# Kernel optimization log

Measured on AMD Instinct MI355X. Metric: run time of the kernel, lower is better.

## Reference

```python
import jax, jax.numpy as jnp
import numpy as np

N = 200_000
E = 6_400_000
EPS = 1e-12


def l2_normalize(x):
    # F.normalize(x, p=2, dim=1): x / max(||x||_2, eps)
    n = jnp.linalg.norm(x, axis=1, keepdims=True)
    return x / jnp.maximum(n, EPS)


def gcn_conv(x, W, b, src, dst, n):
    """PyG GCNConv: add self-loops, symmetric normalization D^-1/2 A D^-1/2,
    linear transform (no bias) on nodes, scatter-add to targets, then + bias."""
    loop = jnp.arange(n)
    s = jnp.concatenate([src, loop])  # sources (messages gathered here)
    d = jnp.concatenate([dst, loop])  # targets (aggregation here)
    deg = jax.ops.segment_sum(jnp.ones(s.shape[0], dtype=x.dtype), d, num_segments=n)
    dinv = jnp.where(deg > 0, jax.lax.rsqrt(deg), 0.0)
    norm = dinv[s] * dinv[d]  # [E+N]
    h = x @ W  # [N, out]
    out = jax.ops.segment_sum(norm[:, None] * h[s], d, num_segments=n)
    return out + b


def setup_inputs() -> dict:
    key = jax.random.key(0)
    ks = jax.random.split(key, 10)
    x = jax.random.normal(ks[0], (N, 3), dtype=jnp.float32)
    edge_index = jax.random.randint(ks[1], (2, E), 0, N, dtype=jnp.int64)

    def glorot(k, shape):
        lim = float(np.sqrt(6.0 / (shape[0] + shape[1])))
        return jax.random.uniform(k, shape, jnp.float32, -lim, lim)

    return {
        "x": x,
        "edge_index": edge_index,
        "W1": glorot(ks[2], (3, 6)),   "b1": jnp.zeros((6,), jnp.float32),
        "W2": glorot(ks[3], (6, 12)),  "b2": jnp.zeros((12,), jnp.float32),
        "W3": glorot(ks[4], (12, 24)), "b3": jnp.zeros((24,), jnp.float32),
        "Wc": glorot(ks[5], (24, 13)), "bc": jnp.zeros((13,), jnp.float32),
    }


def reference(x, edge_index, W1, b1, W2, b2, W3, b3, Wc, bc):
    src, dst = edge_index[0], edge_index[1]
    n = x.shape[0]
    h = jnp.tanh(gcn_conv(x, W1, b1, src, dst, n))
    h = jnp.tanh(l2_normalize(gcn_conv(h, W2, b2, src, dst, n)))
    h = l2_normalize(gcn_conv(h, W3, b3, src, dst, n))
    h = h @ Wc + bc
    return l2_normalize(h)
```

## Files before the change

### kernel.cpp

```cpp
#include <hip/hip_runtime.h>
#include <math.h>


static constexpr int NN = 200000;
static constexpr int NE = 6400000;
static constexpr int BK = 256;

static constexpr int SUBW  = 512;
static constexpr int NBA   = (NN + SUBW - 1) / SUBW;
static constexpr int NBL   = 512;
static constexpr int BKC   = 512;
static constexpr int SEG   = (NE + NBL - 1) / NBL;
static constexpr int SRCSH = 13;
static constexpr int NSB   = (NN + (1 << SRCSH) - 1) >> SRCSH;

static constexpr int S     = 4;
static constexpr int LOGS  = 2;

__global__ void __launch_bounds__(BKC) k_count(const int* __restrict__ dstI,
                                               int* __restrict__ hist, int e) {
  __shared__ int cnt[NBA];
  for (int t = threadIdx.x; t < NBA; t += BKC) cnt[t] = 0;
  __syncthreads();
  int blk = blockIdx.x;
  int st = blk * SEG, en = st + SEG; if (en > e) en = e;
  int i = st + (int)threadIdx.x;
  for (; i + 3 * BKC < en; i += 4 * BKC) {
    int d0 = __builtin_nontemporal_load(dstI + i);
    int d1 = __builtin_nontemporal_load(dstI + i + BKC);
    int d2 = __builtin_nontemporal_load(dstI + i + 2 * BKC);
    int d3 = __builtin_nontemporal_load(dstI + i + 3 * BKC);
    atomicAdd(&cnt[d0 >> 9], 1);
    atomicAdd(&cnt[d1 >> 9], 1);
    atomicAdd(&cnt[d2 >> 9], 1);
    atomicAdd(&cnt[d3 >> 9], 1);
  }
  for (; i < en; i += BKC) {
    int d = __builtin_nontemporal_load(dstI + i);
    atomicAdd(&cnt[d >> 9], 1);
  }
  __syncthreads();
  for (int t = threadIdx.x; t < NBA; t += BKC) hist[(size_t)t * NBL + blk] = cnt[t];
}

__global__ void __launch_bounds__(256) k_scanrow(int* __restrict__ hist,
                                                 int* __restrict__ tot) {
  __shared__ int s0[256], s1[256];
  int b = blockIdx.x, t = threadIdx.x;
  int* row = hist + (size_t)b * NBL;
  int v0 = row[2 * t], v1 = row[2 * t + 1];
  int s = v0 + v1;
  s0[t] = s;
  __syncthreads();
  int* a = s0; int* bb = s1;
  for (int o = 1; o < 256; o <<= 1) {
    bb[t] = a[t] + ((t >= o) ? a[t - o] : 0);
    __syncthreads();
    int* tmp = a; a = bb; bb = tmp;
  }
  int ex = a[t] - s;
  row[2 * t] = ex;
  row[2 * t + 1] = ex + v0;
  if (t == 255) tot[b] = a[t];
}

__global__ void k_scanbin(const int* __restrict__ tot, int* __restrict__ sbase) {
  __shared__ int s0[512], s1[512];
  int t = threadIdx.x;
  int v = (t < NBA) ? tot[t] : 0;
  s0[t] = v;
  __syncthreads();
  int* a = s0; int* b = s1;
  for (int o = 1; o < 512; o <<= 1) {
    b[t] = a[t] + ((t >= o) ? a[t - o] : 0);
    __syncthreads();
    int* tmp = a; a = b; b = tmp;
  }
  if (t < NBA) sbase[t] = a[t] - v;
  if (t == NBA - 1) sbase[NBA] = a[t];
}

__global__ void __launch_bounds__(BKC) k_scat(const int* __restrict__ srcI,
                                              const int* __restrict__ dstI,
                                              const int* __restrict__ hist,
                                              const int* __restrict__ sbase,
                                              unsigned* __restrict__ stg, int e) {
  __shared__ int cur[NBA];
  int blk = blockIdx.x;
  for (int t = threadIdx.x; t < NBA; t += BKC)
    cur[t] = sbase[t] + hist[(size_t)t * NBL + blk];
  __syncthreads();
  int st = blk * SEG, en = st + SEG; if (en > e) en = e;
  int i = st + (int)threadIdx.x;
  for (; i + 3 * BKC < en; i += 4 * BKC) {
    int s0v = __builtin_nontemporal_load(srcI + i);
    int d0 = __builtin_nontemporal_load(dstI + i);
    int s1v = __builtin_nontemporal_load(srcI + i + BKC);
    int d1 = __builtin_nontemporal_load(dstI + i + BKC);
    int s2v = __builtin_nontemporal_load(srcI + i + 2 * BKC);
    int d2 = __builtin_nontemporal_load(dstI + i + 2 * BKC);
    int s3v = __builtin_nontemporal_load(srcI + i + 3 * BKC);
    int d3 = __builtin_nontemporal_load(dstI + i + 3 * BKC);
    int p0 = atomicAdd(&cur[d0 >> 9], 1);
    int p1 = atomicAdd(&cur[d1 >> 9], 1);
    int p2 = atomicAdd(&cur[d2 >> 9], 1);
    int p3 = atomicAdd(&cur[d3 >> 9], 1);
    stg[p0] = ((unsigned)(d0 & (SUBW - 1)) << 18) | (unsigned)s0v;
    stg[p1] = ((unsigned)(d1 & (SUBW - 1)) << 18) | (unsigned)s1v;
    stg[p2] = ((unsigned)(d2 & (SUBW - 1)) << 18) | (unsigned)s2v;
    stg[p3] = ((unsigned)(d3 & (SUBW - 1)) << 18) | (unsigned)s3v;
  }
  for (; i < en; i += BKC) {
    int sv = __builtin_nontemporal_load(srcI + i);
    int d = __builtin_nontemporal_load(dstI + i);
    int p = atomicAdd(&cur[d >> 9], 1);
    stg[p] = ((unsigned)(d & (SUBW - 1)) << 18) | (unsigned)sv;
  }
}

__global__ void __launch_bounds__(BK) k_build(const unsigned* __restrict__ stg,
                                              const int* __restrict__ sbase,
                                              int* __restrict__ rowptr,
                                              int* __restrict__ adj,
                                              int* __restrict__ b8,
                                              int* __restrict__ b13,
                                              int* __restrict__ b17) {
  __shared__ unsigned hist2[SUBW * NSB];
  __shared__ int htot[SUBW];
  __shared__ int s0[SUBW], s1[SUBW];
  int b = blockIdx.x;
  int base = sbase[b];
  int m = sbase[b + 1] - base;
  size_t off = (size_t)base;
  if (b == NBA - 1 && threadIdx.x == 0) rowptr[NN] = base + m;
  for (int t = threadIdx.x; t < SUBW * NSB; t += BK) hist2[t] = 0;
  __syncthreads();
  for (int k = threadIdx.x; k < m; k += BK) {
    unsigned rec = stg[off + k];
    int dl = rec >> 18;
    int sb = (int)((rec & 0x3FFFFu) >> SRCSH);
    atomicAdd(&hist2[dl * NSB + sb], 1u);
  }
  __syncthreads();
  for (int dl = threadIdx.x; dl < SUBW; dl += BK) {
    unsigned run = 0;
    for (int sb = 0; sb < NSB; ++sb) {
      unsigned c = hist2[dl * NSB + sb];
      hist2[dl * NSB + sb] = run;
      run += c;
    }
    htot[dl] = (int)run;
    s0[dl] = (int)run;
  }
  __syncthreads();
  int* a = s0; int* bb = s1;
  for (int o2 = 1; o2 < SUBW; o2 <<= 1) {
    for (int t = threadIdx.x; t < SUBW; t += BK) bb[t] = a[t] + ((t >= o2) ? a[t - o2] : 0);
    __syncthreads();
    int* tmp = a; a = bb; bb = tmp;
  }
  for (int t = threadIdx.x; t < SUBW; t += BK) {
    int node = b * SUBW + t;
    int ex = a[t] - htot[t];
    if (node < NN) {
      rowptr[node] = base + ex;
      b8[node]  = base + ex + (int)hist2[t * NSB + 8];
      b13[node] = base + ex + (int)hist2[t * NSB + 13];
      b17[node] = base + ex + (int)hist2[t * NSB + 17];
    }
    bb[t] = ex;
  }
  __syncthreads();
  for (int k = threadIdx.x; k < m; k += BK) {
    unsigned rec = stg[off + k];
    int dl = rec >> 18;
    unsigned src = rec & 0x3FFFFu;
    int sb = (int)(src >> SRCSH);
    int p = bb[dl] + (int)atomicAdd(&hist2[dl * NSB + sb], 1u);
    adj[base + p] = (int)src;
  }
}

__global__ void k_prep(const float* __restrict__ x, const int* __restrict__ rowptr,
                       float* __restrict__ dinv, float* __restrict__ p1, int n) {
  int i = blockIdx.x * blockDim.x + threadIdx.x;
  if (i >= n) return;
  float di = rsqrtf(1.0f + (float)(rowptr[i + 1] - rowptr[i]));
  dinv[i] = di;
  float3 v;
  v.x = di * x[3 * (size_t)i];
  v.y = di * x[3 * (size_t)i + 1];
  v.z = di * x[3 * (size_t)i + 2];
  *(float3*)(p1 + 3 * (size_t)i) = v;
}

template <int RW> struct RowT;
template <> struct RowT<3> {
  using T = float3;
  static __device__ inline T ld(const float* __restrict__ p) { return *(const float3*)p; }
  static __device__ inline void add(float* __restrict__ a, const T& v) {
    a[0] += v.x; a[1] += v.y; a[2] += v.z;
  }
  static __device__ inline void st(float* __restrict__ p, const float* __restrict__ a) {
    *(float3*)p = make_float3(a[0], a[1], a[2]);
  }
};
template <> struct RowT<6> {
  struct T { float2 a, b, c; };
  static __device__ inline T ld(const float* __restrict__ p) {
    T t; t.a = *(const float2*)p; t.b = *(const float2*)(p + 2); t.c = *(const float2*)(p + 4);
    return t;
  }
  static __device__ inline void add(float* __restrict__ a, const T& v) {
    a[0] += v.a.x; a[1] += v.a.y; a[2] += v.b.x; a[3] += v.b.y; a[4] += v.c.x; a[5] += v.c.y;
  }
  static __device__ inline void st(float* __restrict__ p, const float* __restrict__ a) {
    *(float2*)(p)     = make_float2(a[0], a[1]);
    *(float2*)(p + 2) = make_float2(a[2], a[3]);
    *(float2*)(p + 4) = make_float2(a[4], a[5]);
  }
};
template <> struct RowT<12> {
  struct T { float4 a, b, c; };
  static __device__ inline T ld(const float* __restrict__ p) {
    T t; t.a = *(const float4*)p; t.b = *(const float4*)(p + 4); t.c = *(const float4*)(p + 8);
    return t;
  }
  static __device__ inline void add(float* __restrict__ a, const T& v) {
    a[0] += v.a.x; a[1] += v.a.y; a[2] += v.a.z; a[3] += v.a.w;
    a[4] += v.b.x; a[5] += v.b.y; a[6] += v.b.z; a[7] += v.b.w;
    a[8] += v.c.x; a[9] += v.c.y; a[10] += v.c.z; a[11] += v.c.w;
  }
  static __device__ inline void st(float* __restrict__ p, const float* __restrict__ a) {
    *(float4*)(p)     = make_float4(a[0], a[1], a[2], a[3]);
    *(float4*)(p + 4) = make_float4(a[4], a[5], a[6], a[7]);
    *(float4*)(p + 8) = make_float4(a[8], a[9], a[10], a[11]);
  }
};

template <int RW, int UN>
__device__ inline void gather_p(const int* __restrict__ adj, int st, int en,
                                const float* __restrict__ pin, float* __restrict__ acc,
                                int slot) {
  using RT = RowT<RW>;
  using T = typename RT::T;
  int k = st + slot;
  if (k + (UN - 1) * S < en) {
    int a[UN];
#pragma unroll
    for (int u = 0; u < UN; ++u) a[u] = adj[k + u * S];
    for (;;) {
      int kn = k + UN * S;
      bool more = (kn + (UN - 1) * S < en);
      int b[UN];
#pragma unroll
      for (int u = 0; u < UN; ++u) b[u] = 0;
      if (more) {
#pragma unroll
        for (int u = 0; u < UN; ++u) b[u] = adj[kn + u * S];
      }
      T v[UN];
#pragma unroll
      for (int u = 0; u < UN; ++u) v[u] = RT::ld(pin + (size_t)a[u] * RW);
#pragma unroll
      for (int u = 0; u < UN; ++u) RT::add(acc, v[u]);
      k = kn;
      if (!more) break;
#pragma unroll
      for (int u = 0; u < UN; ++u) a[u] = b[u];
    }
  }
  for (; k < en; k += S) {
    T v = RT::ld(pin + (size_t)adj[k] * RW);
    RT::add(acc, v);
  }
}

template <int FIN>
__device__ inline void group_reduce(float* __restrict__ acc) {
#pragma unroll
  for (int j = 0; j < FIN; ++j) {
    acc[j] += __shfl_xor(acc[j], 1);
    acc[j] += __shfl_xor(acc[j], 2);
  }
}

template <int RW, int FOUT, int MODE>
__global__ void __launch_bounds__(BK, 8) k_gather_fused(
    const int* __restrict__ adj, const int* __restrict__ rowptr,
    const float* __restrict__ pin, const float* __restrict__ W,
    const float* __restrict__ bias, const float* __restrict__ dinv,
    float* __restrict__ pout, int n) {
  __shared__ float sW[RW * FOUT];
  __shared__ float sb[FOUT];
  for (int t = threadIdx.x; t < RW * FOUT; t += BK) sW[t] = W[t];
  if (threadIdx.x < FOUT) sb[threadIdx.x] = bias[threadIdx.x];
  __syncthreads();
  int g = blockIdx.x * blockDim.x + threadIdx.x;
  int i = g >> LOGS;
  int slot = g & (S - 1);
  if (i >= n) return;
  float acc[RW] = {};
  if (slot == 0) {
    typename RowT<RW>::T v = RowT<RW>::ld(pin + (size_t)i * RW);
    RowT<RW>::add(acc, v);
  }
  gather_p<RW, 4>(adj, rowptr[i], rowptr[i + 1], pin, acc, slot);
  group_reduce<RW>(acc);
  float di = dinv[i];
  float h[FOUT];
  float ss = 0.f;
#pragma unroll
  for (int j = 0; j < FOUT; ++j) {
    float s = 0.f;
#pragma unroll
    for (int kk = 0; kk < RW; ++kk) s = fmaf(acc[kk], sW[kk * FOUT + j], s);
    float t = fmaf(di, s, sb[j]);
    h[j] = t;
    ss += t * t;
  }
  float o[FOUT];
  if (MODE == 0) {
#pragma unroll
    for (int j = 0; j < FOUT; ++j) o[j] = di * tanhf(h[j]);
  } else {
    float inv = 1.f / fmaxf(sqrtf(ss), 1e-12f);
#pragma unroll
    for (int j = 0; j < FOUT; ++j) o[j] = di * tanhf(h[j] * inv);
  }
  if (slot == 0) {
    float* po = pout + (size_t)i * FOUT;
    if (MODE == 0) {
      *(float2*)(po)     = make_float2(o[0], o[1]);
      *(float2*)(po + 2) = make_float2(o[2], o[3]);
      *(float2*)(po + 4) = make_float2(o[4], o[5]);
    } else {
      *(float4*)(po)     = make_float4(o[0], o[1], o[2], o[3]);
      *(float4*)(po + 4) = make_float4(o[4], o[5], o[6], o[7]);
      *(float4*)(po + 8) = make_float4(o[8], o[9], o[10], o[11]);
    }
  }
}

template <int RW, bool FIRST>
__global__ void __launch_bounds__(BK, 8) k_gphase(
    const int* __restrict__ adj, const int* __restrict__ stA,
    const int* __restrict__ enB, const float* __restrict__ pin,
    float* __restrict__ accb, int n) {
  int g = blockIdx.x * blockDim.x + threadIdx.x;
  int i = g >> LOGS;
  int slot = g & (S - 1);
  if (i >= n) return;
  float acc[RW] = {};
  if (slot == 0) {
    if (FIRST) {
      typename RowT<RW>::T v = RowT<RW>::ld(pin + (size_t)i * RW);
      RowT<RW>::add(acc, v);
    } else {
      typename RowT<RW>::T v = RowT<RW>::ld(accb + (size_t)i * RW);
      RowT<RW>::add(acc, v);
    }
  }
  gather_p<RW, 4>(adj, stA[i], enB[i], pin, acc, slot);
  group_reduce<RW>(acc);
  if (slot == 0) RowT<RW>::st(accb + (size_t)i * RW, acc);
}

template <int RW, int FOUT, int MODE>
__global__ void __launch_bounds__(BK, 6) k_gphase_last(
    const int* __restrict__ adj, const int* __restrict__ stA,
    const int* __restrict__ rowptr, const float* __restrict__ pin,
    const float* __restrict__ W, const float* __restrict__ bias,
    const float* __restrict__ Wc, const float* __restrict__ bc,
    const float* __restrict__ dinv, const float* __restrict__ accb,
    float* __restrict__ out, int n) {
  constexpr int FC = 13;
  __shared__ float sW[RW * FOUT];
  __shared__ float sb[FOUT];
  __shared__ float sWc[MODE == 2 ? FOUT * FC : 1];
  __shared__ float sbc[MODE == 2 ? FC : 1];
  for (int t = threadIdx.x; t < RW * FOUT; t += BK) sW[t] = W[t];
  if (threadIdx.x < FOUT) sb[threadIdx.x] = bias[threadIdx.x];
  if (MODE == 2) {
    for (int t = threadIdx.x; t < FOUT * FC; t += BK) sWc[t] = Wc[t];
    if (threadIdx.x < FC) sbc[threadIdx.x] = bc[threadIdx.x];
  }
  __syncthreads();
  int g = blockIdx.x * blockDim.x + threadIdx.x;
  int i = g >> LOGS;
  int slot = g & (S - 1);
  if (i >= n) return;
  float acc[RW] = {};
  if (slot == 0) {
    typename RowT<RW>::T v = RowT<RW>::ld(accb + (size_t)i * RW);
    RowT<RW>::add(acc, v);
  }
  gather_p<RW, 4>(adj, stA[i], rowptr[i + 1], pin, acc, slot);
  group_reduce<RW>(acc);
  float di = dinv[i];
  float h[FOUT];
  float ss = 0.f;
#pragma unroll
  for (int j = 0; j < FOUT; ++j) {
    float s = 0.f;
#pragma unroll
    for (int kk = 0; kk < RW; ++kk) s = fmaf(acc[kk], sW[kk * FOUT + j], s);
    float t = fmaf(di, s, sb[j]);
    h[j] = t;
    ss += t * t;
  }
  float inv = 1.f / fmaxf(sqrtf(ss), 1e-12f);
  if (MODE == 1) {
    float o[FOUT];
#pragma unroll
    for (int j = 0; j < FOUT; ++j) o[j] = di * tanhf(h[j] * inv);
    if (slot == 0) {
      float* po = out + (size_t)i * FOUT;
      *(float4*)(po)     = make_float4(o[0], o[1], o[2], o[3]);
      *(float4*)(po + 4) = make_float4(o[4], o[5], o[6], o[7]);
      *(float4*)(po + 8) = make_float4(o[8], o[9], o[10], o[11]);
    }
  } else {
    float v[FC];
    float ss2 = 0.f;
#pragma unroll
    for (int j = 0; j < FC; ++j) {
      float s = sbc[j];
#pragma unroll
      for (int kk = 0; kk < FOUT; ++kk) s = fmaf(h[kk] * inv, sWc[kk * FC + j], s);
      v[j] = s;
      ss2 += s * s;
    }
    float inv2 = 1.f / fmaxf(sqrtf(ss2), 1e-12f);
    if (slot == 0) {
#pragma unroll
      for (int j = 0; j < FC; ++j) out[(size_t)i * FC + j] = v[j] * inv2;
    }
  }
}

extern "C" void kernel_launch(void* const* d_in, const int* in_sizes, int n_in,
                              void* d_out, int out_size, void* d_ws, size_t ws_size,
                              hipStream_t stream) {
  const float* x  = (const float*)d_in[0];
  const int*   ei = (const int*)d_in[1];
  const float* W1 = (const float*)d_in[2];
  const float* b1 = (const float*)d_in[3];
  const float* W2 = (const float*)d_in[4];
  const float* b2 = (const float*)d_in[5];
  const float* W3 = (const float*)d_in[6];
  const float* b3 = (const float*)d_in[7];
  const float* Wc = (const float*)d_in[8];
  const float* bc = (const float*)d_in[9];
  float* out = (float*)d_out;

  const int n = NN;
  const int e = NE;
  const int* srcI = ei;
  const int* dstI = ei + e;

  float* ws = (float*)d_ws;
  float* dinv  = ws;
  int* rowptr  = (int*)(ws + n);
  int* sbase   = rowptr + n + 8;
  int* tot     = sbase + 512;
  int* hist    = tot + 512;
  int* adj     = hist + NBA * NBL;
  int* b8      = adj + e;
  int* b13     = b8 + n;
  int* b17     = b13 + n;
  size_t roff = (size_t)n + (n + 8) + 512 + 512 + (size_t)NBA * NBL + e + 3 * (size_t)n;
  roff = (roff + 15) & ~(size_t)15;
  float* R     = ws + roff;
  unsigned* stg = (unsigned*)R;
  float* p1   = R;
  float* p2   = R + (size_t)3 * n;
  float* p3   = R + (size_t)9 * n;
  float* accb = R + (size_t)21 * n;

  const int gn  = (n + BK - 1) / BK;
  const int gnS = (n * S + BK - 1) / BK;

  k_count<<<NBL, BKC, 0, stream>>>(dstI, hist, e);
  k_scanrow<<<NBA, 256, 0, stream>>>(hist, tot);
  k_scanbin<<<1, 512, 0, stream>>>(tot, sbase);
  k_scat<<<NBL, BKC, 0, stream>>>(srcI, dstI, hist, sbase, stg, e);
  k_build<<<NBA, BK, 0, stream>>>(stg, sbase, rowptr, adj, b8, b13, b17);

  k_prep<<<gn, BK, 0, stream>>>(x, rowptr, dinv, p1, n);

  k_gather_fused<3, 6, 0><<<gnS, BK, 0, stream>>>(adj, rowptr, p1, W1, b1, dinv, p2, n);

  k_gphase<6, true><<<gnS, BK, 0, stream>>>(adj, rowptr, b13, p2, accb, n);
  k_gphase_last<6, 12, 1><<<gnS, BK, 0, stream>>>(adj, b13, rowptr, p2, W2, b2,
                                                  Wc, bc, dinv, accb, p3, n);

  k_gphase<12, true><<<gnS, BK, 0, stream>>>(adj, rowptr, b8, p3, accb, n);
  k_gphase<12, false><<<gnS, BK, 0, stream>>>(adj, b8, b17, p3, accb, n);
  k_gphase_last<12, 24, 2><<<gnS, BK, 0, stream>>>(adj, b17, rowptr, p3, W3, b3,
                                                   Wc, bc, dinv, accb, out, n);
}
```

Baseline: 457.5 us.

## Split CSR build blocks in half and stage adjacency writes in LDS

```diff
diff --git a/kernel.cpp b/kernel.cpp
--- a/kernel.cpp
+++ b/kernel.cpp
@@ -8,9 +8,11 @@
 
 static constexpr int SUBW  = 512;
 static constexpr int NBA   = (NN + SUBW - 1) / SUBW;
-static constexpr int NBL   = 512;
+static constexpr int NBB   = 2 * NBA;
+static constexpr int NBL   = 1024;
 static constexpr int BKC   = 512;
 static constexpr int SEG   = (NE + NBL - 1) / NBL;
+static constexpr int LCAP  = 8832;
 static constexpr int SRCSH = 13;
 static constexpr int NSB   = (NN + (1 << SRCSH) - 1) >> SRCSH;
 
@@ -48,8 +50,9 @@
   __shared__ int s0[256], s1[256];
   int b = blockIdx.x, t = threadIdx.x;
   int* row = hist + (size_t)b * NBL;
-  int v0 = row[2 * t], v1 = row[2 * t + 1];
-  int s = v0 + v1;
+  uint4 vv = ((const uint4*)row)[t];
+  int v0 = (int)vv.x, v1 = (int)vv.y, v2 = (int)vv.z, v3 = (int)vv.w;
+  int s = v0 + v1 + v2 + v3;
   s0[t] = s;
   __syncthreads();
   int* a = s0; int* bb = s1;
@@ -59,8 +62,12 @@
     int* tmp = a; a = bb; bb = tmp;
   }
   int ex = a[t] - s;
-  row[2 * t] = ex;
-  row[2 * t + 1] = ex + v0;
+  uint4 w;
+  w.x = (unsigned)ex;
+  w.y = (unsigned)(ex + v0);
+  w.z = (unsigned)(ex + v0 + v1);
+  w.w = (unsigned)(ex + v0 + v1 + v2);
+  ((uint4*)row)[t] = w;
   if (t == 255) tot[b] = a[t];
 }
 
@@ -125,24 +132,29 @@
                                               int* __restrict__ b8,
                                               int* __restrict__ b13,
                                               int* __restrict__ b17) {
-  __shared__ unsigned hist2[SUBW * NSB];
-  __shared__ int htot[SUBW];
-  __shared__ int s0[SUBW], s1[SUBW];
-  int b = blockIdx.x;
-  int base = sbase[b];
-  int m = sbase[b + 1] - base;
+  __shared__ unsigned hist2[256 * NSB];
+  __shared__ int htot[256];
+  __shared__ int s0[256], s1[256];
+  __shared__ unsigned astg[LCAP];
+  int b2 = blockIdx.x;
+  int bin = b2 >> 1, half = b2 & 1;
+  int base = sbase[bin];
+  int m = sbase[bin + 1] - base;
   size_t off = (size_t)base;
-  if (b == NBA - 1 && threadIdx.x == 0) rowptr[NN] = base + m;
-  for (int t = threadIdx.x; t < SUBW * NSB; t += BK) hist2[t] = 0;
+  if (b2 == 0 && threadIdx.x == 0) rowptr[NN] = sbase[NBA];
+  for (int t = threadIdx.x; t < 256 * NSB; t += BK) hist2[t] = 0;
   __syncthreads();
   for (int k = threadIdx.x; k < m; k += BK) {
     unsigned rec = stg[off + k];
-    int dl = rec >> 18;
-    int sb = (int)((rec & 0x3FFFFu) >> SRCSH);
-    atomicAdd(&hist2[dl * NSB + sb], 1u);
-  }
-  __syncthreads();
-  for (int dl = threadIdx.x; dl < SUBW; dl += BK) {
+    int dl = (int)(rec >> 18);
+    if ((dl >> 8) == half) {
+      int sb = (int)((rec & 0x3FFFFu) >> SRCSH);
+      atomicAdd(&hist2[(dl & 255) * NSB + sb], 1u);
+    }
+  }
+  __syncthreads();
+  {
+    int dl = threadIdx.x;
     unsigned run = 0;
     for (int sb = 0; sb < NSB; ++sb) {
       unsigned c = hist2[dl * NSB + sb];
@@ -154,31 +166,40 @@
   }
   __syncthreads();
   int* a = s0; int* bb = s1;
-  for (int o2 = 1; o2 < SUBW; o2 <<= 1) {
-    for (int t = threadIdx.x; t < SUBW; t += BK) bb[t] = a[t] + ((t >= o2) ? a[t - o2] : 0);
+  for (int o2 = 1; o2 < 256; o2 <<= 1) {
+    int t = threadIdx.x;
+    bb[t] = a[t] + ((t >= o2) ? a[t - o2] : 0);
     __syncthreads();
     int* tmp = a; a = bb; bb = tmp;
   }
-  for (int t = threadIdx.x; t < SUBW; t += BK) {
-    int node = b * SUBW + t;
+  int mytot = a[255];
+  int base_eff = base + (half ? (m - mytot) : 0);
+  {
+    int t = threadIdx.x;
+    int node = bin * SUBW + half * 256 + t;
     int ex = a[t] - htot[t];
     if (node < NN) {
-      rowptr[node] = base + ex;
-      b8[node]  = base + ex + (int)hist2[t * NSB + 8];
-      b13[node] = base + ex + (int)hist2[t * NSB + 13];
-      b17[node] = base + ex + (int)hist2[t * NSB + 17];
+      rowptr[node] = base_eff + ex;
+      b8[node]  = base_eff + ex + (int)hist2[t * NSB + 8];
+      b13[node] = base_eff + ex + (int)hist2[t * NSB + 13];
+      b17[node] = base_eff + ex + (int)hist2[t * NSB + 17];
     }
     bb[t] = ex;
   }
   __syncthreads();
   for (int k = threadIdx.x; k < m; k += BK) {
     unsigned rec = stg[off + k];
-    int dl = rec >> 18;
+    int dl = (int)(rec >> 18);
+    if ((dl >> 8) != half) continue;
     unsigned src = rec & 0x3FFFFu;
     int sb = (int)(src >> SRCSH);
-    int p = bb[dl] + (int)atomicAdd(&hist2[dl * NSB + sb], 1u);
-    adj[base + p] = (int)src;
-  }
+    int p = bb[dl & 255] + (int)atomicAdd(&hist2[(dl & 255) * NSB + sb], 1u);
+    if (p < LCAP) astg[p] = src;
+    else adj[base_eff + p] = (int)src;
+  }
+  __syncthreads();
+  int mm = mytot < LCAP ? mytot : LCAP;
+  for (int k = threadIdx.x; k < mm; k += BK) adj[base_eff + k] = (int)astg[k];
 }
 
 __global__ void k_prep(const float* __restrict__ x, const int* __restrict__ rowptr,
@@ -485,7 +506,7 @@
   k_scanrow<<<NBA, 256, 0, stream>>>(hist, tot);
   k_scanbin<<<1, 512, 0, stream>>>(tot, sbase);
   k_scat<<<NBL, BKC, 0, stream>>>(srcI, dstI, hist, sbase, stg, e);
-  k_build<<<NBA, BK, 0, stream>>>(stg, sbase, rowptr, adj, b8, b13, b17);
+  k_build<<<NBB, BK, 0, stream>>>(stg, sbase, rowptr, adj, b8, b13, b17);
 
   k_prep<<<gn, BK, 0, stream>>>(x, rowptr, dinv, p1, n);
 
```

Result: slower. 466.8 us (+2.0%).
